# Optimization experiments

Measured on AMD Instinct MI355X. Metric: run time of the kernel, lower is better.

The kernel has to match this reference:

```python
import jax, jax.numpy as jnp
import numpy as np


def setup_inputs() -> dict:
    key = jax.random.key(0)
    k1, k2, k3 = jax.random.split(key, 3)
    B, C, H, W = 16, 256, 128, 128
    r = 16  # channels // reduction
    x = jax.random.normal(k1, (B, C, H, W), dtype=jnp.float32)
    # 1x1 conv kernels flattened to linear weights (fan-in scaled init)
    w1 = jax.random.normal(k2, (r, C), dtype=jnp.float32) * (1.0 / np.sqrt(C))
    b1 = jnp.zeros((r,), dtype=jnp.float32)
    w2 = jax.random.normal(k3, (C, r), dtype=jnp.float32) * (1.0 / np.sqrt(r))
    b2 = jnp.zeros((C,), dtype=jnp.float32)
    return {"x": x, "w1": w1, "b1": b1, "w2": w2, "b2": b2}


def reference(x, w1, b1, w2, b2):
    b, c, h, w = x.shape
    n = h * w
    x_flat = x.reshape(b, c, n)
    mu = x_flat.mean(axis=2, keepdims=True)
    xc = x_flat - mu  # [b, c, n]
    # v[b,i] = mean_j cov[b,i,j] where cov = xc @ xc^T / (n-1).
    # Algebraic reassociation: mean_j sum_k xc[i,k] xc[j,k] = sum_k xc[i,k] * s[k] / c
    # with s[k] = sum_j xc[j,k]. Avoids the O(C^2 * n) bmm; same math.
    s = xc.sum(axis=1)  # [b, n]
    denom = jnp.float32(max(1, n - 1) * c)
    v = jnp.einsum('bcn,bn->bc', xc, s) / denom  # [b, c]
    # MLP of 1x1 convs on a [b,c,1,1] descriptor == two linear layers
    h1 = jax.nn.relu(v @ w1.T + b1)              # [b, r]
    gate = jax.nn.sigmoid(h1 @ w2.T + b2)        # [b, c]
    return x * gate[:, :, None, None]
```

## Files before the change

kernel.cpp:

```cpp
#include <hip/hip_runtime.h>
#include <hip/hip_bf16.h>

#define B_ 16
#define C_ 256
#define N_ 16384
#define WT_ 256
#define TPB_ 64
#define R16_ 16
#define TLSTR_ 129

typedef float f32x4 __attribute__((ext_vector_type(4)));

__device__ __forceinline__ float4 ldf4(const float* p) {
    return *reinterpret_cast<const float4*>(p);
}
__device__ __forceinline__ float bfl(unsigned p) {
    return __uint_as_float(p << 16);
}
__device__ __forceinline__ float bfh(unsigned p) {
    return __uint_as_float(p & 0xFFFF0000u);
}

__global__ __launch_bounds__(1024)
void kA(const float* __restrict__ x,
        float* __restrict__ Ppart,
        float* __restrict__ RSpart) {
    extern __shared__ ushort tl[];
    __shared__ float4 csp[16][64];
    __shared__ float colsum[WT_];
    __shared__ float2 pq[3][C_];

    const int tile = blockIdx.x;
    const int b = blockIdx.y;
    const int t = threadIdx.x;
    const int lane = t & 63;
    const int w = t >> 6;

    const float* xt = x + (size_t)b * C_ * N_ + tile * WT_ + (lane << 2);
    const int c0 = w << 4;

    float4 cs = make_float4(0.f, 0.f, 0.f, 0.f);
#pragma unroll
    for (int k = 0; k < 16; ++k) {
        const int c = c0 + k;
        float4 v = ldf4(xt + (size_t)c * N_);
        cs.x += v.x; cs.y += v.y; cs.z += v.z; cs.w += v.w;
        __hip_bfloat162 lo = __float22bfloat162_rn(make_float2(v.x, v.y));
        __hip_bfloat162 hi = __float22bfloat162_rn(make_float2(v.z, v.w));
        unsigned* dst = reinterpret_cast<unsigned*>(tl) + c * TLSTR_ + (lane << 1);
        dst[0] = *reinterpret_cast<unsigned*>(&lo);
        dst[1] = *reinterpret_cast<unsigned*>(&hi);
    }
    csp[w][lane] = cs;
    __syncthreads();

    if (t < WT_) {
        const float* base = reinterpret_cast<const float*>(&csp[0][t >> 2]) + (t & 3);
        float s = 0.f;
#pragma unroll
        for (int w2 = 0; w2 < 16; ++w2) s += base[w2 * 256];
        colsum[t] = s;
    }
    __syncthreads();

    const int c = t & 255, q = t >> 8;
    const unsigned* row = reinterpret_cast<const unsigned*>(tl) + c * TLSTR_ + (q << 5);
    const float* csq = colsum + (q << 6);
    float P = 0.f, RS = 0.f;
#pragma unroll
    for (int j = 0; j < 32; ++j) {
        const unsigned pk = row[j];
        const float vx = bfl(pk), vy = bfh(pk);
        P += vx * csq[2 * j] + vy * csq[2 * j + 1];
        RS += vx + vy;
    }
    if (q) pq[q - 1][c] = make_float2(P, RS);
    __syncthreads();
    if (t < C_) {
        P  += pq[0][t].x + pq[1][t].x + pq[2][t].x;
        RS += pq[0][t].y + pq[1][t].y + pq[2][t].y;
        const size_t base = ((size_t)b * TPB_ + tile) * C_;
        Ppart [base + t] = P;
        RSpart[base + t] = RS;
    }
}

__global__ void kB(const float* __restrict__ Ppart,
                   const float* __restrict__ RSpart,
                   const float* __restrict__ w1, const float* __restrict__ b1,
                   const float* __restrict__ w2, const float* __restrict__ b2,
                   float* __restrict__ gate) {
    const int b = blockIdx.x;
    const int t = threadIdx.x;

    float P = 0.f, RS = 0.f;
#pragma unroll 8
    for (int k = 0; k < TPB_; ++k) {
        P  += Ppart [((size_t)b * TPB_ + k) * C_ + t];
        RS += RSpart[((size_t)b * TPB_ + k) * C_ + t];
    }

    __shared__ float red[4];
    float s = RS;
#pragma unroll
    for (int off = 32; off; off >>= 1) s += __shfl_down(s, off, 64);
    if ((t & 63) == 0) red[t >> 6] = s;
    __syncthreads();
    const float T = red[0] + red[1] + red[2] + red[3];
    const float M = T / (float)N_;
    const float denom = (float)(N_ - 1) * (float)C_;

    __shared__ float vl[C_];
    vl[t] = (P - M * RS) / denom;
    __syncthreads();

    __shared__ float hpart[R16_][16];
    __shared__ float h1[R16_];
    {
        const int i = t >> 4, cc = t & 15;
        float a = 0.f;
#pragma unroll
        for (int k = 0; k < 16; ++k)
            a += vl[(cc << 4) + k] * w1[i * C_ + (cc << 4) + k];
        hpart[i][cc] = a;
    }
    __syncthreads();
    if (t < R16_) {
        float a = b1[t];
#pragma unroll
        for (int k = 0; k < 16; ++k) a += hpart[t][k];
        h1[t] = a > 0.f ? a : 0.f;
    }
    __syncthreads();

    float a = b2[t];
#pragma unroll
    for (int i = 0; i < R16_; ++i) a += h1[i] * w2[t * R16_ + i];
    gate[b * C_ + t] = 1.f / (1.f + __expf(-a));
}

__global__ void kC(const float* __restrict__ x,
                   const float* __restrict__ gate,
                   float* __restrict__ out) {
    const int nrows = B_ * C_;
    for (int row = blockIdx.x; row < nrows; row += gridDim.x) {
        const int rr = nrows - 1 - row;
        const float g = gate[rr];
        const float4* src = reinterpret_cast<const float4*>(x) + (size_t)rr * 4096;
        f32x4* dst = reinterpret_cast<f32x4*>(out) + (size_t)rr * 4096;
        for (int i = threadIdx.x; i < 4096; i += blockDim.x) {
            float4 vx = src[i];
            f32x4 r;
            r.x = vx.x * g; r.y = vx.y * g; r.z = vx.z * g; r.w = vx.w * g;
            __builtin_nontemporal_store(r, dst + i);
        }
    }
}

extern "C" void kernel_launch(void* const* d_in, const int* in_sizes, int n_in,
                              void* d_out, int out_size, void* d_ws, size_t ws_size,
                              hipStream_t stream) {
    (void)in_sizes; (void)n_in; (void)out_size; (void)ws_size;
    const float* x  = (const float*)d_in[0];
    const float* w1 = (const float*)d_in[1];
    const float* b1 = (const float*)d_in[2];
    const float* w2 = (const float*)d_in[3];
    const float* b2 = (const float*)d_in[4];
    float* out = (float*)d_out;

    float* ws     = (float*)d_ws;
    float* Ppart  = ws;
    float* RSpart = Ppart + (size_t)B_ * TPB_ * C_;
    float* gate   = RSpart + (size_t)B_ * TPB_ * C_;

    const int tl_bytes = C_ * (2 * TLSTR_) * (int)sizeof(ushort);
    static bool attr_done = false;
    if (!attr_done) {
        hipFuncSetAttribute((const void*)kA,
                            hipFuncAttributeMaxDynamicSharedMemorySize,
                            tl_bytes);
        attr_done = true;
    }

    hipLaunchKernelGGL(kA, dim3(TPB_, B_), dim3(1024), tl_bytes, stream,
                       x, Ppart, RSpart);
    hipLaunchKernelGGL(kB, dim3(B_), dim3(256), 0, stream,
                       Ppart, RSpart, w1, b1, w2, b2, gate);
    hipLaunchKernelGGL(kC, dim3(2048), dim3(256), 0, stream,
                       x, gate, out);
}
```

Measured before the change: 138.8 us.

## Halve kA tile width and block size to raise occupancy

The stats kernel kA now processes 128-column tiles with 512-thread blocks instead of 256 columns with 1024 threads. Its bf16 transpose tile moves to static shared memory of about 66 KB, and the column-sum and partial reductions are restructured to match. The smaller footprint is meant to let several blocks share a CU, giving more memory parallelism and better latency hiding on the 256 MB read. The cost is twice as many partial rows for kB to reduce and more blocks overall.

Result: no change. 139.6 us (+0.6%).

```diff
diff --git a/kernel.cpp b/kernel.cpp
--- a/kernel.cpp
+++ b/kernel.cpp
@@ -4,10 +4,10 @@
 #define B_ 16
 #define C_ 256
 #define N_ 16384
-#define WT_ 256
-#define TPB_ 64
+#define WT_ 128
+#define TPB_ 128
 #define R16_ 16
-#define TLSTR_ 129
+#define TLSTR_ 66
 
 typedef float f32x4 __attribute__((ext_vector_type(4)));
 
@@ -21,51 +21,58 @@
     return __uint_as_float(p & 0xFFFF0000u);
 }
 
-__global__ __launch_bounds__(1024)
+__global__ __launch_bounds__(512, 4)
 void kA(const float* __restrict__ x,
         float* __restrict__ Ppart,
         float* __restrict__ RSpart) {
-    extern __shared__ ushort tl[];
-    __shared__ float4 csp[16][64];
+    __shared__ unsigned tl[C_ * TLSTR_];
+    __shared__ float4 csp[8][2][32];
     __shared__ float colsum[WT_];
-    __shared__ float2 pq[3][C_];
+    __shared__ float2 phalf[C_];
 
     const int tile = blockIdx.x;
     const int b = blockIdx.y;
     const int t = threadIdx.x;
     const int lane = t & 63;
     const int w = t >> 6;
+    const int h = lane >> 5;
+    const int ln = lane & 31;
 
-    const float* xt = x + (size_t)b * C_ * N_ + tile * WT_ + (lane << 2);
-    const int c0 = w << 4;
+    const float* xt = x + (size_t)b * C_ * N_ + tile * WT_ + (ln << 2);
+    const int c0 = (w << 5) + h;
 
     float4 cs = make_float4(0.f, 0.f, 0.f, 0.f);
 #pragma unroll
     for (int k = 0; k < 16; ++k) {
-        const int c = c0 + k;
+        const int c = c0 + (k << 1);
         float4 v = ldf4(xt + (size_t)c * N_);
         cs.x += v.x; cs.y += v.y; cs.z += v.z; cs.w += v.w;
         __hip_bfloat162 lo = __float22bfloat162_rn(make_float2(v.x, v.y));
         __hip_bfloat162 hi = __float22bfloat162_rn(make_float2(v.z, v.w));
-        unsigned* dst = reinterpret_cast<unsigned*>(tl) + c * TLSTR_ + (lane << 1);
+        unsigned* dst = tl + c * TLSTR_ + (ln << 1);
         dst[0] = *reinterpret_cast<unsigned*>(&lo);
         dst[1] = *reinterpret_cast<unsigned*>(&hi);
     }
-    csp[w][lane] = cs;
+    csp[w][h][ln] = cs;
     __syncthreads();
 
-    if (t < WT_) {
-        const float* base = reinterpret_cast<const float*>(&csp[0][t >> 2]) + (t & 3);
-        float s = 0.f;
+    if (t < 32) {
+        float4 s = make_float4(0.f, 0.f, 0.f, 0.f);
 #pragma unroll
-        for (int w2 = 0; w2 < 16; ++w2) s += base[w2 * 256];
-        colsum[t] = s;
+        for (int w2 = 0; w2 < 8; ++w2) {
+#pragma unroll
+            for (int h2 = 0; h2 < 2; ++h2) {
+                float4 p = csp[w2][h2][t];
+                s.x += p.x; s.y += p.y; s.z += p.z; s.w += p.w;
+            }
+        }
+        *reinterpret_cast<float4*>(&colsum[t << 2]) = s;
     }
     __syncthreads();
 
-    const int c = t & 255, q = t >> 8;
-    const unsigned* row = reinterpret_cast<const unsigned*>(tl) + c * TLSTR_ + (q << 5);
-    const float* csq = colsum + (q << 6);
+    const int c = t & 255, hh = t >> 8;
+    const unsigned* row = tl + c * TLSTR_ + (hh << 5);
+    const float* csq = colsum + (hh << 6);
     float P = 0.f, RS = 0.f;
 #pragma unroll
     for (int j = 0; j < 32; ++j) {
@@ -74,11 +81,11 @@
         P += vx * csq[2 * j] + vy * csq[2 * j + 1];
         RS += vx + vy;
     }
-    if (q) pq[q - 1][c] = make_float2(P, RS);
+    if (hh) phalf[c] = make_float2(P, RS);
     __syncthreads();
     if (t < C_) {
-        P  += pq[0][t].x + pq[1][t].x + pq[2][t].x;
-        RS += pq[0][t].y + pq[1][t].y + pq[2][t].y;
+        P += phalf[t].x;
+        RS += phalf[t].y;
         const size_t base = ((size_t)b * TPB_ + tile) * C_;
         Ppart [base + t] = P;
         RSpart[base + t] = RS;
@@ -173,16 +180,7 @@
     float* RSpart = Ppart + (size_t)B_ * TPB_ * C_;
     float* gate   = RSpart + (size_t)B_ * TPB_ * C_;
 
-    const int tl_bytes = C_ * (2 * TLSTR_) * (int)sizeof(ushort);
-    static bool attr_done = false;
-    if (!attr_done) {
-        hipFuncSetAttribute((const void*)kA,
-                            hipFuncAttributeMaxDynamicSharedMemorySize,
-                            tl_bytes);
-        attr_done = true;
-    }
-
-    hipLaunchKernelGGL(kA, dim3(TPB_, B_), dim3(1024), tl_bytes, stream,
+    hipLaunchKernelGGL(kA, dim3(TPB_, B_), dim3(512), 0, stream,
                        x, Ppart, RSpart);
     hipLaunchKernelGGL(kB, dim3(B_), dim3(256), 0, stream,
                        Ppart, RSpart, w1, b1, w2, b2, gate);
```
